# Kernel tuning notes

Hardware: AMD Instinct MI355X
Metric: run time of the kernel (lower is better)

## Reference

```python
import jax, jax.numpy as jnp
import numpy as np

NT, NL, D = 200000, 50000, 128
ETA, EREV, ELL, ELBL = 1000000, 1000000, 500000, 500000


def setup_inputs() -> dict:
    key = jax.random.key(0)
    ks = jax.random.split(key, 17)
    s = 1.0 / np.sqrt(D)
    return {
        "x_title": jax.random.normal(ks[0], (NT, D), jnp.float32),
        "label_embed": jax.random.normal(ks[1], (NL, D), jnp.float32),
        "W_l_tl": jax.random.normal(ks[2], (D, D), jnp.float32) * s,
        "b_l_tl": jnp.zeros((D,), jnp.float32),
        "W_r_tl": jax.random.normal(ks[3], (D, D), jnp.float32) * s,
        "W_l_ll": jax.random.normal(ks[4], (D, D), jnp.float32) * s,
        "b_l_ll": jnp.zeros((D,), jnp.float32),
        "W_r_ll": jax.random.normal(ks[5], (D, D), jnp.float32) * s,
        "label_node_id": jnp.arange(NL, dtype=jnp.int64),
        "ta_src": jax.random.randint(ks[6], (ETA,), 0, NT, jnp.int64),
        "ta_dst": jax.random.randint(ks[7], (ETA,), 0, NL, jnp.int64),
        "rev_src": jax.random.randint(ks[8], (EREV,), 0, NL, jnp.int64),
        "rev_dst": jax.random.randint(ks[9], (EREV,), 0, NT, jnp.int64),
        "ll_src": jax.random.randint(ks[10], (ELL,), 0, NL, jnp.int64),
        "ll_dst": jax.random.randint(ks[11], (ELL,), 0, NL, jnp.int64),
        "el_src": jax.random.randint(ks[12], (ELBL,), 0, NT, jnp.int64),
        "el_dst": jax.random.randint(ks[13], (ELBL,), 0, NL, jnp.int64),
    }


def sage_conv(x_src, x_dst, src, dst, W_l, b_l, W_r, n_dst):
    """PyG SAGEConv (mean aggr): lin_l(mean_j x_src[j]) + lin_r(x_dst). lin_r has no bias."""
    msg = x_src[src]                                              # [E, D] gather
    agg = jax.ops.segment_sum(msg, dst, num_segments=n_dst)       # [n_dst, D]
    cnt = jax.ops.segment_sum(jnp.ones((src.shape[0],), x_src.dtype), dst, num_segments=n_dst)
    agg = agg / jnp.maximum(cnt, 1.0)[:, None]
    return agg @ W_l.T + b_l + x_dst @ W_r.T


def reference(x_title, label_embed, W_l_tl, b_l_tl, W_r_tl, W_l_ll, b_l_ll, W_r_ll,
              label_node_id, ta_src, ta_dst, rev_src, rev_dst, ll_src, ll_dst, el_src, el_dst):
    x_label = label_embed[label_node_id]                          # [NL, D]
    # HeteroConv with aggr='sum': sum SAGEConv outputs per destination node type
    out_label = (sage_conv(x_title, x_label, ta_src, ta_dst, W_l_tl, b_l_tl, W_r_tl, x_label.shape[0])
                 + sage_conv(x_label, x_label, ll_src, ll_dst, W_l_ll, b_l_ll, W_r_ll, x_label.shape[0]))
    out_title = sage_conv(x_label, x_title, rev_src, rev_dst, W_l_tl, b_l_tl, W_r_tl, x_title.shape[0])
    out_title = jax.nn.relu(out_title)
    out_label = jax.nn.relu(out_label)
    # dot-product classifier over supervision edges
    pred = (out_title[el_src] * out_label[el_dst]).sum(axis=-1)   # [ELBL]
    return pred, out_title, out_label
```

## Files before the change

kernel.cpp:

```cpp
#include <hip/hip_runtime.h>

#define D     128
#define NT    200000
#define NL    50000
#define ETA   1000000
#define EREV  1000000
#define ELL   500000
#define ELBL  500000
#define DD    (D * D)

#define NBK   256
#define CH    8192
#define NCH_TA  ((ETA  + CH - 1) / CH)
#define NCH_LL  ((ELL  + CH - 1) / CH)
#define NCH_REV ((EREV + CH - 1) / CH)
#define R_TA  ((NL + NBK - 1) / NBK)
#define R_LL  R_TA
#define R_REV ((NT + NBK - 1) / NBK)
#define RMAX  800

typedef __attribute__((ext_vector_type(8))) __bf16 bf16x8;
typedef __attribute__((ext_vector_type(4))) float f32x4;
typedef __attribute__((ext_vector_type(2))) _Float16 f16x2;
typedef __attribute__((ext_vector_type(4))) _Float16 f16x4;
typedef __attribute__((ext_vector_type(8))) _Float16 f16x8;

__device__ inline bf16x8 cvt8(float4 a, float4 b)
{
    bf16x8 r;
    r[0] = (__bf16)a.x; r[1] = (__bf16)a.y; r[2] = (__bf16)a.z; r[3] = (__bf16)a.w;
    r[4] = (__bf16)b.x; r[5] = (__bf16)b.y; r[6] = (__bf16)b.z; r[7] = (__bf16)b.w;
    return r;
}

__device__ inline f16x8 pack8(const f32x4& a, const f32x4& b)
{
    f16x8 o;
    o[0] = (_Float16)a[0]; o[1] = (_Float16)a[1];
    o[2] = (_Float16)a[2]; o[3] = (_Float16)a[3];
    o[4] = (_Float16)b[0]; o[5] = (_Float16)b[1];
    o[6] = (_Float16)b[2]; o[7] = (_Float16)b[3];
    return o;
}


__global__ __launch_bounds__(256) void prep_weights(
    const float* __restrict__ Wl_tl, const float* __restrict__ Wr_tl,
    const float* __restrict__ Wl_ll, const float* __restrict__ Wr_ll,
    const float* __restrict__ b_tl, const float* __restrict__ b_ll,
    __bf16* __restrict__ Wb, float* __restrict__ bias_sum)
{
    int i = blockIdx.x * 256 + threadIdx.x;
    if (i < DD) {
        int n = i >> 7, k = i & 127;
        int kc = k >> 5, q = (k >> 3) & 3, j = k & 7;
        int nt = n >> 4, m15 = n & 15;
        int dst = (((kc * 8 + nt) * 4 + q) * 16 + m15) * 8 + j;
        Wb[dst]          = (__bf16)Wl_tl[i];
        Wb[DD + dst]     = (__bf16)Wr_tl[i];
        Wb[2 * DD + dst] = (__bf16)Wl_ll[i];
        Wb[3 * DD + dst] = (__bf16)(Wr_tl[i] + Wr_ll[i]);
    }
    if (i < D) bias_sum[i] = b_tl[i] + b_ll[i];
}

__global__ __launch_bounds__(256) void part_count(
    const int* __restrict__ taD, const int* __restrict__ llD,
    const int* __restrict__ revD,
    int* __restrict__ MTa, int* __restrict__ MLl, int* __restrict__ MRev)
{
    __shared__ int h[NBK];
    int bb = blockIdx.x, tid = threadIdx.x;
    const int* dst; int E, R, chunk; int* M;
    if (bb < NCH_TA) { dst = taD; E = ETA; R = R_TA; M = MTa; chunk = bb; }
    else if (bb < NCH_TA + NCH_LL) { dst = llD; E = ELL; R = R_LL; M = MLl; chunk = bb - NCH_TA; }
    else { dst = revD; E = EREV; R = R_REV; M = MRev; chunk = bb - NCH_TA - NCH_LL; }

    h[tid] = 0;
    __syncthreads();
    int eBeg = chunk * CH, eEnd = min(E, eBeg + CH);
    for (int e = eBeg + tid; e < eEnd; e += 256)
        atomicAdd(&h[dst[e] / R], 1);
    __syncthreads();
    M[chunk * NBK + tid] = h[tid];
}

__global__ __launch_bounds__(256) void part_scan(
    int* __restrict__ MTa, int* __restrict__ MLl, int* __restrict__ MRev,
    int* __restrict__ bsTa, int* __restrict__ bsLl, int* __restrict__ bsRev)
{
    int rel = blockIdx.x, tid = threadIdx.x;
    int* M; int nCh; int* bs;
    if (rel == 0) { M = MTa; nCh = NCH_TA; bs = bsTa; }
    else if (rel == 1) { M = MLl; nCh = NCH_LL; bs = bsLl; }
    else { M = MRev; nCh = NCH_REV; bs = bsRev; }

    int run = 0;
    for (int c = 0; c < nCh; ++c) {
        int v = M[c * NBK + tid];
        M[c * NBK + tid] = run;
        run += v;
    }
    int lane = tid & 63, w = tid >> 6;
    int incl = run;
#pragma unroll
    for (int off = 1; off < 64; off <<= 1) {
        int v = __shfl_up(incl, off, 64);
        if (lane >= off) incl += v;
    }
    __shared__ int ws[4];
    if (lane == 63) ws[w] = incl;
    __syncthreads();
    int base = 0;
    for (int j = 0; j < w; ++j) base += ws[j];
    int excl = base + incl - run;
    bs[tid] = excl;
    if (tid == 255) bs[NBK] = excl + run;
}

__global__ __launch_bounds__(256) void part_scatter(
    const int* __restrict__ taS, const int* __restrict__ taD,
    const int* __restrict__ llS, const int* __restrict__ llD,
    const int* __restrict__ revS, const int* __restrict__ revD,
    const int* __restrict__ MTa, const int* __restrict__ MLl,
    const int* __restrict__ MRev,
    const int* __restrict__ bsTa, const int* __restrict__ bsLl,
    const int* __restrict__ bsRev,
    int2* __restrict__ pTa, int2* __restrict__ pLl, int2* __restrict__ pRev)
{
    __shared__ int cur[NBK];
    int bb = blockIdx.x, tid = threadIdx.x;
    const int *src, *dst, *M, *bs; int E, R, chunk; int2* pr;
    if (bb < NCH_TA) {
        src = taS; dst = taD; M = MTa; bs = bsTa; pr = pTa;
        E = ETA; R = R_TA; chunk = bb;
    } else if (bb < NCH_TA + NCH_LL) {
        src = llS; dst = llD; M = MLl; bs = bsLl; pr = pLl;
        E = ELL; R = R_LL; chunk = bb - NCH_TA;
    } else {
        src = revS; dst = revD; M = MRev; bs = bsRev; pr = pRev;
        E = EREV; R = R_REV; chunk = bb - NCH_TA - NCH_LL;
    }
    cur[tid] = bs[tid] + M[chunk * NBK + tid];
    __syncthreads();
    int eBeg = chunk * CH, eEnd = min(E, eBeg + CH);
    for (int e = eBeg + tid; e < eEnd; e += 256) {
        int d = dst[e], s = src[e];
        int pos = atomicAdd(&cur[d / R], 1);
        pr[pos] = make_int2(s, d);
    }
}

__global__ __launch_bounds__(256) void csr_build(
    const int2* __restrict__ pTa, const int* __restrict__ bsTa,
    int* __restrict__ cntTa, int* __restrict__ curTa, int* __restrict__ csrTa,
    const int2* __restrict__ pLl, const int* __restrict__ bsLl,
    int* __restrict__ cntLl, int* __restrict__ curLl, int* __restrict__ csrLl,
    const int2* __restrict__ pRev, const int* __restrict__ bsRev,
    int* __restrict__ cntRev, int* __restrict__ curRev, int* __restrict__ csrRev)
{
    __shared__ int counts[RMAX];
    __shared__ int starts[RMAX];
    __shared__ int ws[4];
    int bb = blockIdx.x, tid = threadIdx.x;
    const int2* pr; const int* bs; int *cnt, *cur, *csr; int R, n;
    if (bb < NBK) {
        pr = pTa; bs = bsTa; cnt = cntTa; cur = curTa; csr = csrTa;
        R = R_TA; n = NL;
    } else if (bb < 2 * NBK) {
        bb -= NBK;
        pr = pLl; bs = bsLl; cnt = cntLl; cur = curLl; csr = csrLl;
        R = R_LL; n = NL;
    } else {
        bb -= 2 * NBK;
        pr = pRev; bs = bsRev; cnt = cntRev; cur = curRev; csr = csrRev;
        R = R_REV; n = NT;
    }
    const int rowBase = bb * R;
    const int eBeg = bs[bb], eEnd = bs[bb + 1];
    const int K = (R + 255) / 256;

    for (int k = 0; k < K; ++k) {
        int r = tid * K + k;
        if (r < R) counts[r] = 0;
    }
    __syncthreads();
    for (int e = eBeg + tid; e < eEnd; e += 256)
        atomicAdd(&counts[pr[e].y - rowBase], 1);
    __syncthreads();

    int local[4]; int sum = 0;
    for (int k = 0; k < K; ++k) {
        int r = tid * K + k;
        int v = (r < R) ? counts[r] : 0;
        local[k] = sum;
        sum += v;
    }
    int lane = tid & 63, w = tid >> 6;
    int incl = sum;
#pragma unroll
    for (int off = 1; off < 64; off <<= 1) {
        int v = __shfl_up(incl, off, 64);
        if (lane >= off) incl += v;
    }
    if (lane == 63) ws[w] = incl;
    __syncthreads();
    int wbase = 0;
    for (int j = 0; j < w; ++j) wbase += ws[j];
    int tbase = wbase + incl - sum;

    for (int k = 0; k < K; ++k) {
        int r = tid * K + k;
        if (r < R) {
            int v = counts[r];
            int excl = tbase + local[k];
            starts[r] = excl;
            int row = rowBase + r;
            if (row < n) {
                cnt[row] = v;
                cur[row] = eBeg + excl + v;
            }
        }
    }
    __syncthreads();

    for (int e = eBeg + tid; e < eEnd; e += 256) {
        int2 p = pr[e];
        int pos = eBeg + atomicAdd(&starts[p.y - rowBase], 1);
        csr[pos] = p.x;
    }
}

__global__ __launch_bounds__(256) void agg_rev_kernel(
    const _Float16* __restrict__ Z, const int* __restrict__ csr,
    const int* __restrict__ cnt, const int* __restrict__ cur,
    float* __restrict__ outF)
{
    int row = blockIdx.x * 4 + (threadIdx.x >> 6);
    if (row >= NT) return;
    int lane = threadIdx.x & 63;
    int deg = cnt[row];
    int end = cur[row];
    int e = end - deg;
    float ax = 0.f, ay = 0.f;
    for (; e + 3 < end; e += 4) {
        int s0 = csr[e], s1 = csr[e + 1], s2 = csr[e + 2], s3 = csr[e + 3];
        f16x2 v0 = *reinterpret_cast<const f16x2*>(Z + (size_t)s0 * D + lane * 2);
        f16x2 v1 = *reinterpret_cast<const f16x2*>(Z + (size_t)s1 * D + lane * 2);
        f16x2 v2 = *reinterpret_cast<const f16x2*>(Z + (size_t)s2 * D + lane * 2);
        f16x2 v3 = *reinterpret_cast<const f16x2*>(Z + (size_t)s3 * D + lane * 2);
        ax += (float)v0[0] + (float)v1[0] + (float)v2[0] + (float)v3[0];
        ay += (float)v0[1] + (float)v1[1] + (float)v2[1] + (float)v3[1];
    }
    for (; e < end; ++e) {
        int s0 = csr[e];
        f16x2 v0 = *reinterpret_cast<const f16x2*>(Z + (size_t)s0 * D + lane * 2);
        ax += (float)v0[0];
        ay += (float)v0[1];
    }
    float r = 1.0f / fmaxf((float)deg, 1.0f);
    *reinterpret_cast<float2*>(outF + (size_t)row * D + lane * 2) =
        make_float2(ax * r, ay * r);
}

#define BTA ((NL + 3) / 4)
__global__ __launch_bounds__(256) void agg_ta_ll_kernel(
    const _Float16* __restrict__ Zta, const int* __restrict__ csrTa,
    const int* __restrict__ cntTa, const int* __restrict__ curTa,
    _Float16* __restrict__ meanTa,
    const _Float16* __restrict__ Zll, const int* __restrict__ csrLl,
    const int* __restrict__ cntLl, const int* __restrict__ curLl,
    _Float16* __restrict__ meanLl)
{
    int b = blockIdx.x;
    const _Float16* Z; const int *csr, *cnt, *cur; _Float16* o;
    if (b < BTA) { Z = Zta; csr = csrTa; cnt = cntTa; cur = curTa; o = meanTa; }
    else { b -= BTA; Z = Zll; csr = csrLl; cnt = cntLl; cur = curLl; o = meanLl; }
    int row = b * 4 + (threadIdx.x >> 6);
    if (row >= NL) return;
    int lane = threadIdx.x & 63;
    int deg = cnt[row];
    int end = cur[row];
    int e = end - deg;
    float ax = 0.f, ay = 0.f;
    for (; e + 3 < end; e += 4) {
        int s0 = csr[e], s1 = csr[e + 1], s2 = csr[e + 2], s3 = csr[e + 3];
        f16x2 v0 = *reinterpret_cast<const f16x2*>(Z + (size_t)s0 * D + lane * 2);
        f16x2 v1 = *reinterpret_cast<const f16x2*>(Z + (size_t)s1 * D + lane * 2);
        f16x2 v2 = *reinterpret_cast<const f16x2*>(Z + (size_t)s2 * D + lane * 2);
        f16x2 v3 = *reinterpret_cast<const f16x2*>(Z + (size_t)s3 * D + lane * 2);
        ax += (float)v0[0] + (float)v1[0] + (float)v2[0] + (float)v3[0];
        ay += (float)v0[1] + (float)v1[1] + (float)v2[1] + (float)v3[1];
    }
    for (; e < end; ++e) {
        int s0 = csr[e];
        f16x2 v0 = *reinterpret_cast<const f16x2*>(Z + (size_t)s0 * D + lane * 2);
        ax += (float)v0[0];
        ay += (float)v0[1];
    }
    float r = 1.0f / fmaxf((float)deg, 1.0f);
    f16x2 ov; ov[0] = (_Float16)(ax * r); ov[1] = (_Float16)(ay * r);
    *reinterpret_cast<f16x2*>(o + (size_t)row * D + lane * 2) = ov;
}

__global__ __launch_bounds__(256) void z_label_gemm(
    const float* __restrict__ labelEmbed, const int* __restrict__ labelNodeId,
    const __bf16* __restrict__ Wb,
    _Float16* __restrict__ Zrev, _Float16* __restrict__ Zll)
{
    __shared__ __bf16 sW[2 * DD];
    const int tid = threadIdx.x;
    const int lane = tid & 63;
    const int m15 = lane & 15, q = lane >> 4;
    const int rowOrig = blockIdx.x * 64 + (tid >> 6) * 16 + m15;
    const int row = (rowOrig < NL) ? rowOrig : NL - 1;
    const int xr = labelNodeId[row];

    const float* pe = labelEmbed + (size_t)xr * D + q * 8;
    float4 xf[8];
#pragma unroll
    for (int kc = 0; kc < 4; ++kc) {
        xf[2 * kc]     = *reinterpret_cast<const float4*>(pe + kc * 32);
        xf[2 * kc + 1] = *reinterpret_cast<const float4*>(pe + kc * 32 + 4);
    }
    {
        const float4* g0 = reinterpret_cast<const float4*>(Wb);
        const float4* g2 = reinterpret_cast<const float4*>(Wb + 2 * DD);
        float4* ls = reinterpret_cast<float4*>(sW);
        for (int it = tid; it < 2048; it += 256) {
            ls[it] = g0[it];
            ls[2048 + it] = g2[it];
        }
    }
    bf16x8 aE[4];
#pragma unroll
    for (int kc = 0; kc < 4; ++kc) aE[kc] = cvt8(xf[2 * kc], xf[2 * kc + 1]);
    __syncthreads();

    const bf16x8* wl = reinterpret_cast<const bf16x8*>(sW);
    const f32x4 z4 = {0.f, 0.f, 0.f, 0.f};
#pragma unroll
    for (int pass = 0; pass < 2; ++pass) {
        const int sb = pass ? 2048 : 0;
        _Float16* Z = pass ? Zll : Zrev;
        f32x4 acc[8];
#pragma unroll
        for (int nt = 0; nt < 8; ++nt) acc[nt] = z4;
#pragma unroll
        for (int kc = 0; kc < 4; ++kc)
#pragma unroll
            for (int nt = 0; nt < 8; ++nt)
                acc[nt] = __builtin_amdgcn_mfma_f32_16x16x32_bf16(
                    wl[sb + (kc * 8 + nt) * 64 + lane], aE[kc], acc[nt], 0, 0, 0);
        if (rowOrig < NL) {
            f16x8* zp = reinterpret_cast<f16x8*>(Z + (size_t)row * D + q * 32);
#pragma unroll
            for (int k = 0; k < 4; ++k)
                zp[k] = pack8(acc[2 * k], acc[2 * k + 1]);
        }
    }
}

__global__ __launch_bounds__(256) void gemm_title_mfma(
    const float* __restrict__ xTitle, const __bf16* __restrict__ Wb,
    const float* __restrict__ b_tl,
    _Float16* __restrict__ Zta, _Float16* __restrict__ Zot,
    float* outTitle )
{
    __shared__ __bf16 sW[2 * DD];
    const int tid = threadIdx.x;
    const int lane = tid & 63;
    const int m15 = lane & 15, q = lane >> 4;
    const int row = blockIdx.x * 64 + (tid >> 6) * 16 + m15;

    const float* px = xTitle + (size_t)row * D + q * 8;
    float4 xf[8];
#pragma unroll
    for (int kc = 0; kc < 4; ++kc) {
        xf[2 * kc]     = *reinterpret_cast<const float4*>(px + kc * 32);
        xf[2 * kc + 1] = *reinterpret_cast<const float4*>(px + kc * 32 + 4);
    }
    {
        const float4* gs = reinterpret_cast<const float4*>(Wb);
        float4* ls = reinterpret_cast<float4*>(sW);
        for (int it = tid; it < 4096; it += 256) ls[it] = gs[it];
    }
    bf16x8 aX[4];
#pragma unroll
    for (int kc = 0; kc < 4; ++kc) aX[kc] = cvt8(xf[2 * kc], xf[2 * kc + 1]);

    f32x4 mr[8];
    {
        const f32x4* mp = reinterpret_cast<const f32x4*>(outTitle + (size_t)row * D + q * 32);
#pragma unroll
        for (int c = 0; c < 8; ++c) mr[c] = mp[c];
    }
    __syncthreads();

    const bf16x8* wl = reinterpret_cast<const bf16x8*>(sW);
    const f32x4 z4 = {0.f, 0.f, 0.f, 0.f};
    f32x4 acc[8];

#pragma unroll
    for (int nt = 0; nt < 8; ++nt) acc[nt] = z4;
#pragma unroll
    for (int kc = 0; kc < 4; ++kc)
#pragma unroll
        for (int nt = 0; nt < 8; ++nt)
            acc[nt] = __builtin_amdgcn_mfma_f32_16x16x32_bf16(
                wl[(kc * 8 + nt) * 64 + lane], aX[kc], acc[nt], 0, 0, 0);
    {
        f16x8* zp = reinterpret_cast<f16x8*>(Zta + (size_t)row * D + q * 32);
#pragma unroll
        for (int k = 0; k < 4; ++k)
            zp[k] = pack8(acc[2 * k], acc[2 * k + 1]);
    }

#pragma unroll
    for (int nt = 0; nt < 8; ++nt) acc[nt] = z4;
#pragma unroll
    for (int kc = 0; kc < 4; ++kc)
#pragma unroll
        for (int nt = 0; nt < 8; ++nt)
            acc[nt] = __builtin_amdgcn_mfma_f32_16x16x32_bf16(
                wl[2048 + (kc * 8 + nt) * 64 + lane], aX[kc], acc[nt], 0, 0, 0);
#pragma unroll
    for (int c = 0; c < 8; ++c) {
        acc[c][0] += mr[c][0]; acc[c][1] += mr[c][1];
        acc[c][2] += mr[c][2]; acc[c][3] += mr[c][3];
    }
#pragma unroll
    for (int nt = 0; nt < 8; ++nt) {
        float4 bb = *reinterpret_cast<const float4*>(b_tl + nt * 16 + q * 4);
        acc[nt][0] = fmaxf(acc[nt][0] + bb.x, 0.0f);
        acc[nt][1] = fmaxf(acc[nt][1] + bb.y, 0.0f);
        acc[nt][2] = fmaxf(acc[nt][2] + bb.z, 0.0f);
        acc[nt][3] = fmaxf(acc[nt][3] + bb.w, 0.0f);
        *reinterpret_cast<f32x4*>(outTitle + (size_t)row * D + nt * 16 + q * 4) = acc[nt];
    }
    if (Zot) {
        f16x8* zp = reinterpret_cast<f16x8*>(Zot + (size_t)row * D + q * 32);
#pragma unroll
        for (int k = 0; k < 4; ++k)
            zp[k] = pack8(acc[2 * k], acc[2 * k + 1]);
    }
}

__global__ __launch_bounds__(256) void gemm_label_mfma(
    const float* __restrict__ labelEmbed, const int* __restrict__ labelNodeId,
    const __bf16* __restrict__ Wb, const float* __restrict__ bias_sum,
    const _Float16* __restrict__ meanTa, const _Float16* __restrict__ meanLl,
    float* __restrict__ outLabel, _Float16* __restrict__ Zol)
{
    __shared__ __bf16 sW[DD];
    const int tid = threadIdx.x;
    const int lane = tid & 63;
    const int m15 = lane & 15, q = lane >> 4;
    const int rowOrig = blockIdx.x * 64 + (tid >> 6) * 16 + m15;
    const int row = (rowOrig < NL) ? rowOrig : NL - 1;
    const int xr = labelNodeId[row];

    const float* pe = labelEmbed + (size_t)xr * D + q * 8;
    float4 xf[8];
#pragma unroll
    for (int kc = 0; kc < 4; ++kc) {
        xf[2 * kc]     = *reinterpret_cast<const float4*>(pe + kc * 32);
        xf[2 * kc + 1] = *reinterpret_cast<const float4*>(pe + kc * 32 + 4);
    }
    {
        const float4* g3 = reinterpret_cast<const float4*>(Wb + 3 * DD);
        float4* ls = reinterpret_cast<float4*>(sW);
        for (int it = tid; it < 2048; it += 256) ls[it] = g3[it];
    }
    bf16x8 aXl[4];
#pragma unroll
    for (int kc = 0; kc < 4; ++kc) aXl[kc] = cvt8(xf[2 * kc], xf[2 * kc + 1]);

    f16x8 mt[4], ml[4];
    {
        const f16x8* pt = reinterpret_cast<const f16x8*>(meanTa + (size_t)row * D + q * 32);
        const f16x8* pl = reinterpret_cast<const f16x8*>(meanLl + (size_t)row * D + q * 32);
#pragma unroll
        for (int k = 0; k < 4; ++k) { mt[k] = pt[k]; ml[k] = pl[k]; }
    }
    __syncthreads();

    const bf16x8* wl = reinterpret_cast<const bf16x8*>(sW);
    const f32x4 z4 = {0.f, 0.f, 0.f, 0.f};
    f32x4 acc[8];
#pragma unroll
    for (int nt = 0; nt < 8; ++nt) acc[nt] = z4;
#pragma unroll
    for (int kc = 0; kc < 4; ++kc)
#pragma unroll
        for (int nt = 0; nt < 8; ++nt)
            acc[nt] = __builtin_amdgcn_mfma_f32_16x16x32_bf16(
                wl[(kc * 8 + nt) * 64 + lane], aXl[kc], acc[nt], 0, 0, 0);

#pragma unroll
    for (int k = 0; k < 4; ++k) {
#pragma unroll
        for (int h = 0; h < 8; ++h) {
            int j = k * 8 + h;
            acc[j >> 2][j & 3] += (float)mt[k][h] + (float)ml[k][h];
        }
    }
#pragma unroll
    for (int nt = 0; nt < 8; ++nt) {
        float4 bb = *reinterpret_cast<const float4*>(bias_sum + nt * 16 + q * 4);
        acc[nt][0] = fmaxf(acc[nt][0] + bb.x, 0.0f);
        acc[nt][1] = fmaxf(acc[nt][1] + bb.y, 0.0f);
        acc[nt][2] = fmaxf(acc[nt][2] + bb.z, 0.0f);
        acc[nt][3] = fmaxf(acc[nt][3] + bb.w, 0.0f);
    }
    if (rowOrig < NL) {
#pragma unroll
        for (int nt = 0; nt < 8; ++nt)
            *reinterpret_cast<f32x4*>(outLabel + (size_t)row * D + nt * 16 + q * 4) = acc[nt];
        f16x8* zp = reinterpret_cast<f16x8*>(Zol + (size_t)row * D + q * 32);
#pragma unroll
        for (int k = 0; k < 4; ++k)
            zp[k] = pack8(acc[2 * k], acc[2 * k + 1]);
    }
}

__global__ __launch_bounds__(256) void pred_kernel(
    const _Float16* __restrict__ Zot, const float* __restrict__ outTitle,
    const _Float16* __restrict__ Zol,
    const int* __restrict__ elSrc, const int* __restrict__ elDst,
    float* __restrict__ pred, int E)
{
    int idx = blockIdx.x * 256 + threadIdx.x;
    int e = idx >> 5;
    if (e >= E) return;
    int l = idx & 31;
    int s = elSrc[e];
    int d = elDst[e];
    f16x4 b = *reinterpret_cast<const f16x4*>(Zol + (size_t)d * D + l * 4);
    float v;
    if (Zot) {
        f16x4 a = *reinterpret_cast<const f16x4*>(Zot + (size_t)s * D + l * 4);
        v = (float)a[0] * (float)b[0] + (float)a[1] * (float)b[1]
          + (float)a[2] * (float)b[2] + (float)a[3] * (float)b[3];
    } else {
        const float* at = outTitle + (size_t)s * D + (l & 7) * 16 + (l >> 3) * 4;
        float4 a = *reinterpret_cast<const float4*>(at);
        v = a.x * (float)b[0] + a.y * (float)b[1]
          + a.z * (float)b[2] + a.w * (float)b[3];
    }
#pragma unroll
    for (int off = 16; off > 0; off >>= 1) v += __shfl_down(v, off, 32);
    if (l == 0) pred[e] = v;
}

extern "C" void kernel_launch(void* const* d_in, const int* in_sizes, int n_in,
                              void* d_out, int out_size, void* d_ws, size_t ws_size,
                              hipStream_t stream)
{
    const float* x_title       = (const float*)d_in[0];
    const float* label_embed   = (const float*)d_in[1];
    const float* W_l_tl        = (const float*)d_in[2];
    const float* b_l_tl        = (const float*)d_in[3];
    const float* W_r_tl        = (const float*)d_in[4];
    const float* W_l_ll        = (const float*)d_in[5];
    const float* b_l_ll        = (const float*)d_in[6];
    const float* W_r_ll        = (const float*)d_in[7];
    const int*   label_node_id = (const int*)d_in[8];
    const int*   ta_src        = (const int*)d_in[9];
    const int*   ta_dst        = (const int*)d_in[10];
    const int*   rev_src       = (const int*)d_in[11];
    const int*   rev_dst       = (const int*)d_in[12];
    const int*   ll_src        = (const int*)d_in[13];
    const int*   ll_dst        = (const int*)d_in[14];
    const int*   el_src        = (const int*)d_in[15];
    const int*   el_dst        = (const int*)d_in[16];

    float* out       = (float*)d_out;
    float* pred      = out;
    float* out_title = out + ELBL;
    float* out_label = out_title + (size_t)NT * D;

    char* p = (char*)d_ws;
    __bf16*   Wb      = (__bf16*)p;            p += (size_t)4 * DD * sizeof(__bf16);
    float*    bias_sum= (float*)p;             p += D * sizeof(float);
    _Float16* Zta     = (_Float16*)p;          p += (size_t)NT * D * sizeof(_Float16);
    _Float16* Zrev    = Zta;
    _Float16* Zll     = (_Float16*)p;          p += (size_t)NL * D * sizeof(_Float16);
    _Float16* Zol     = Zll;
    _Float16* meanTa  = (_Float16*)p;          p += (size_t)NL * D * sizeof(_Float16);
    _Float16* meanLl  = (_Float16*)p;          p += (size_t)NL * D * sizeof(_Float16);
    int2*     pTa     = (int2*)meanTa;
    int2*     pLl     = (int2*)(pTa + ETA);
    int2*     pRev    = (int2*)(pLl + ELL);
    int*      cntTa   = (int*)p;               p += NL * sizeof(int);
    int*      cntLl   = (int*)p;               p += NL * sizeof(int);
    int*      cntRev  = (int*)p;               p += NT * sizeof(int);
    int*      curTa   = (int*)p;               p += NL * sizeof(int);
    int*      curLl   = (int*)p;               p += NL * sizeof(int);
    int*      curRev  = (int*)p;               p += NT * sizeof(int);
    int*      csrTa   = (int*)p;               p += ETA * sizeof(int);
    int*      csrLl   = (int*)p;               p += ELL * sizeof(int);
    int*      csrRev  = (int*)p;               p += EREV * sizeof(int);
    int*      MTa     = (int*)p;               p += (size_t)NCH_TA * NBK * sizeof(int);
    int*      MLl     = (int*)p;               p += (size_t)NCH_LL * NBK * sizeof(int);
    int*      MRev    = (int*)p;               p += (size_t)NCH_REV * NBK * sizeof(int);
    int*      bsTa    = (int*)p;               p += (NBK + 1) * sizeof(int);
    int*      bsLl    = (int*)p;               p += (NBK + 1) * sizeof(int);
    int*      bsRev   = (int*)p;               p += (NBK + 1) * sizeof(int);
    _Float16* Zot     = (_Float16*)p;          p += (size_t)NT * D * sizeof(_Float16);
    if ((size_t)(p - (char*)d_ws) > ws_size) Zot = nullptr;

    prep_weights<<<(DD + 255) / 256, 256, 0, stream>>>(
        W_l_tl, W_r_tl, W_l_ll, W_r_ll, b_l_tl, b_l_ll, Wb, bias_sum);

    z_label_gemm<<<(NL + 63) / 64, 256, 0, stream>>>(
        label_embed, label_node_id, Wb, Zrev, Zll);

    part_count<<<NCH_TA + NCH_LL + NCH_REV, 256, 0, stream>>>(
        ta_dst, ll_dst, rev_dst, MTa, MLl, MRev);
    part_scan<<<3, 256, 0, stream>>>(MTa, MLl, MRev, bsTa, bsLl, bsRev);
    part_scatter<<<NCH_TA + NCH_LL + NCH_REV, 256, 0, stream>>>(
        ta_src, ta_dst, ll_src, ll_dst, rev_src, rev_dst,
        MTa, MLl, MRev, bsTa, bsLl, bsRev, pTa, pLl, pRev);
    csr_build<<<3 * NBK, 256, 0, stream>>>(
        pTa, bsTa, cntTa, curTa, csrTa,
        pLl, bsLl, cntLl, curLl, csrLl,
        pRev, bsRev, cntRev, curRev, csrRev);

    agg_rev_kernel<<<NT / 4, 256, 0, stream>>>(
        Zrev, csrRev, cntRev, curRev, out_title);

    gemm_title_mfma<<<NT / 64, 256, 0, stream>>>(
        x_title, Wb, b_l_tl, Zta, Zot, out_title);

    agg_ta_ll_kernel<<<2 * BTA, 256, 0, stream>>>(
        Zta, csrTa, cntTa, curTa, meanTa,
        Zll, csrLl, cntLl, curLl, meanLl);

    gemm_label_mfma<<<(NL + 63) / 64, 256, 0, stream>>>(
        label_embed, label_node_id, Wb, bias_sum, meanTa, meanLl,
        out_label, Zol);

    pred_kernel<<<(ELBL * 32) / 256, 256, 0, stream>>>(
        Zot, out_title, Zol, el_src, el_dst, pred, ELBL);
}
```

Baseline: 659.0 us.

## Split rev aggregation across feature halves and double GEMM block size

```diff
diff --git a/kernel.cpp b/kernel.cpp
--- a/kernel.cpp
+++ b/kernel.cpp
@@ -231,36 +231,35 @@
     }
 }
 
+#define HREV ((NT + 3) / 4)
 __global__ __launch_bounds__(256) void agg_rev_kernel(
     const _Float16* __restrict__ Z, const int* __restrict__ csr,
     const int* __restrict__ cnt, const int* __restrict__ cur,
     float* __restrict__ outF)
 {
-    int row = blockIdx.x * 4 + (threadIdx.x >> 6);
+    int bb = blockIdx.x;
+    int half = (bb >= HREV);
+    if (half) bb -= HREV;
+    int row = bb * 4 + (threadIdx.x >> 6);
     if (row >= NT) return;
     int lane = threadIdx.x & 63;
+    int c = half * 64 + lane;
     int deg = cnt[row];
     int end = cur[row];
     int e = end - deg;
-    float ax = 0.f, ay = 0.f;
+    float ax = 0.f;
     for (; e + 3 < end; e += 4) {
         int s0 = csr[e], s1 = csr[e + 1], s2 = csr[e + 2], s3 = csr[e + 3];
-        f16x2 v0 = *reinterpret_cast<const f16x2*>(Z + (size_t)s0 * D + lane * 2);
-        f16x2 v1 = *reinterpret_cast<const f16x2*>(Z + (size_t)s1 * D + lane * 2);
-        f16x2 v2 = *reinterpret_cast<const f16x2*>(Z + (size_t)s2 * D + lane * 2);
-        f16x2 v3 = *reinterpret_cast<const f16x2*>(Z + (size_t)s3 * D + lane * 2);
-        ax += (float)v0[0] + (float)v1[0] + (float)v2[0] + (float)v3[0];
-        ay += (float)v0[1] + (float)v1[1] + (float)v2[1] + (float)v3[1];
-    }
-    for (; e < end; ++e) {
-        int s0 = csr[e];
-        f16x2 v0 = *reinterpret_cast<const f16x2*>(Z + (size_t)s0 * D + lane * 2);
-        ax += (float)v0[0];
-        ay += (float)v0[1];
-    }
+        float v0 = (float)Z[(size_t)s0 * D + c];
+        float v1 = (float)Z[(size_t)s1 * D + c];
+        float v2 = (float)Z[(size_t)s2 * D + c];
+        float v3 = (float)Z[(size_t)s3 * D + c];
+        ax += v0 + v1 + v2 + v3;
+    }
+    for (; e < end; ++e)
+        ax += (float)Z[(size_t)csr[e] * D + c];
     float r = 1.0f / fmaxf((float)deg, 1.0f);
-    *reinterpret_cast<float2*>(outF + (size_t)row * D + lane * 2) =
-        make_float2(ax * r, ay * r);
+    outF[(size_t)row * D + c] = ax * r;
 }
 
 #define BTA ((NL + 3) / 4)
@@ -303,7 +302,7 @@
     *reinterpret_cast<f16x2*>(o + (size_t)row * D + lane * 2) = ov;
 }
 
-__global__ __launch_bounds__(256) void z_label_gemm(
+__global__ __launch_bounds__(512) void z_label_gemm(
     const float* __restrict__ labelEmbed, const int* __restrict__ labelNodeId,
     const __bf16* __restrict__ Wb,
     _Float16* __restrict__ Zrev, _Float16* __restrict__ Zll)
@@ -312,7 +311,7 @@
     const int tid = threadIdx.x;
     const int lane = tid & 63;
     const int m15 = lane & 15, q = lane >> 4;
-    const int rowOrig = blockIdx.x * 64 + (tid >> 6) * 16 + m15;
+    const int rowOrig = blockIdx.x * 128 + (tid >> 6) * 16 + m15;
     const int row = (rowOrig < NL) ? rowOrig : NL - 1;
     const int xr = labelNodeId[row];
 
@@ -327,7 +326,7 @@
         const float4* g0 = reinterpret_cast<const float4*>(Wb);
         const float4* g2 = reinterpret_cast<const float4*>(Wb + 2 * DD);
         float4* ls = reinterpret_cast<float4*>(sW);
-        for (int it = tid; it < 2048; it += 256) {
+        for (int it = tid; it < 2048; it += 512) {
             ls[it] = g0[it];
             ls[2048 + it] = g2[it];
         }
@@ -361,7 +360,7 @@
     }
 }
 
-__global__ __launch_bounds__(256) void gemm_title_mfma(
+__global__ __launch_bounds__(512) void gemm_title_mfma(
     const float* __restrict__ xTitle, const __bf16* __restrict__ Wb,
     const float* __restrict__ b_tl,
     _Float16* __restrict__ Zta, _Float16* __restrict__ Zot,
@@ -371,7 +370,8 @@
     const int tid = threadIdx.x;
     const int lane = tid & 63;
     const int m15 = lane & 15, q = lane >> 4;
-    const int row = blockIdx.x * 64 + (tid >> 6) * 16 + m15;
+    const int rowOrig = blockIdx.x * 128 + (tid >> 6) * 16 + m15;
+    const int row = (rowOrig < NT) ? rowOrig : NT - 1;
 
     const float* px = xTitle + (size_t)row * D + q * 8;
     float4 xf[8];
@@ -383,7 +383,7 @@
     {
         const float4* gs = reinterpret_cast<const float4*>(Wb);
         float4* ls = reinterpret_cast<float4*>(sW);
-        for (int it = tid; it < 4096; it += 256) ls[it] = gs[it];
+        for (int it = tid; it < 4096; it += 512) ls[it] = gs[it];
     }
     bf16x8 aX[4];
 #pragma unroll
@@ -409,7 +409,7 @@
         for (int nt = 0; nt < 8; ++nt)
             acc[nt] = __builtin_amdgcn_mfma_f32_16x16x32_bf16(
                 wl[(kc * 8 + nt) * 64 + lane], aX[kc], acc[nt], 0, 0, 0);
-    {
+    if (rowOrig < NT) {
         f16x8* zp = reinterpret_cast<f16x8*>(Zta + (size_t)row * D + q * 32);
 #pragma unroll
         for (int k = 0; k < 4; ++k)
@@ -436,13 +436,17 @@
         acc[nt][1] = fmaxf(acc[nt][1] + bb.y, 0.0f);
         acc[nt][2] = fmaxf(acc[nt][2] + bb.z, 0.0f);
         acc[nt][3] = fmaxf(acc[nt][3] + bb.w, 0.0f);
-        *reinterpret_cast<f32x4*>(outTitle + (size_t)row * D + nt * 16 + q * 4) = acc[nt];
-    }
-    if (Zot) {
-        f16x8* zp = reinterpret_cast<f16x8*>(Zot + (size_t)row * D + q * 32);
-#pragma unroll
-        for (int k = 0; k < 4; ++k)
-            zp[k] = pack8(acc[2 * k], acc[2 * k + 1]);
+    }
+    if (rowOrig < NT) {
+#pragma unroll
+        for (int nt = 0; nt < 8; ++nt)
+            *reinterpret_cast<f32x4*>(outTitle + (size_t)row * D + nt * 16 + q * 4) = acc[nt];
+        if (Zot) {
+            f16x8* zp = reinterpret_cast<f16x8*>(Zot + (size_t)row * D + q * 32);
+#pragma unroll
+            for (int k = 0; k < 4; ++k)
+                zp[k] = pack8(acc[2 * k], acc[2 * k + 1]);
+        }
     }
 }
 
@@ -613,7 +617,7 @@
     prep_weights<<<(DD + 255) / 256, 256, 0, stream>>>(
         W_l_tl, W_r_tl, W_l_ll, W_r_ll, b_l_tl, b_l_ll, Wb, bias_sum);
 
-    z_label_gemm<<<(NL + 63) / 64, 256, 0, stream>>>(
+    z_label_gemm<<<(NL + 127) / 128, 512, 0, stream>>>(
         label_embed, label_node_id, Wb, Zrev, Zll);
 
     part_count<<<NCH_TA + NCH_LL + NCH_REV, 256, 0, stream>>>(
@@ -627,10 +631,10 @@
         pLl, bsLl, cntLl, curLl, csrLl,
         pRev, bsRev, cntRev, curRev, csrRev);
 
-    agg_rev_kernel<<<NT / 4, 256, 0, stream>>>(
+    agg_rev_kernel<<<2 * HREV, 256, 0, stream>>>(
         Zrev, csrRev, cntRev, curRev, out_title);
 
-    gemm_title_mfma<<<NT / 64, 256, 0, stream>>>(
+    gemm_title_mfma<<<(NT + 127) / 128, 512, 0, stream>>>(
         x_title, Wb, b_l_tl, Zta, Zot, out_title);
 
     agg_ta_ll_kernel<<<2 * BTA, 256, 0, stream>>>(
```

Result: slower. 705.8 us (+7.1%).
